# Kernel optimization log

Hardware: AMD Instinct MI355X
Metric: run time of the kernel (lower is better)

## Reference

```python
import jax, jax.numpy as jnp
import numpy as np

B, NVIS, NHID, NCLASS = 2048, 2048, 1024, 64


def setup_inputs() -> dict:
    key = jax.random.key(0)
    k1, k2, k3, k4, k5 = jax.random.split(key, 5)
    return {
        "v": jax.random.normal(k1, (B, NVIS), dtype=jnp.float32),
        "W": jax.random.normal(k2, (NVIS, NHID), dtype=jnp.float32),
        "c": jax.random.normal(k3, (1, NHID), dtype=jnp.float32),
        "d": jax.random.normal(k4, (1, NCLASS), dtype=jnp.float32),
        "U": jax.random.normal(k5, (NCLASS, NHID), dtype=jnp.float32),
    }


def reference(v, W, c, d, U):
    # precomputed_factor: [B, nhid]
    pre = jnp.matmul(v, W) + c
    # class free energies F[b, y] = d[0, y] + sum_j softplus(pre[b, j] + U[y, j])
    # broadcast to [B, nclass, nhid], reduce over hidden units
    F = d[0] + jnp.sum(jax.nn.softplus(pre[:, None, :] + U[None, :, :]), axis=-1)  # [B, nclass]
    # pairwise normalization 1 / sum_d exp(F_d - F_c) == softmax(F) along classes
    class_probs = jax.nn.softmax(F, axis=1)
    max_idx = jnp.argmax(class_probs, axis=1)
    one_hot = jax.nn.one_hot(max_idx, U.shape[0], dtype=jnp.int32)
    return class_probs, one_hot
```

## Files before the change

kernel.cpp:

```cpp
#include <hip/hip_runtime.h>

constexpr int kB    = 2048;
constexpr int kVIS  = 2048;
constexpr int kHID  = 1024;
constexpr int kCLS  = 64;
constexpr float kLog2e = 1.4426950408889634f;

typedef __attribute__((ext_vector_type(8))) short bf16x8;
typedef __attribute__((ext_vector_type(4))) float f32x4;

__device__ __forceinline__ unsigned short f2bf(float x) {
    unsigned u = __float_as_uint(x);
    u += 0x7fffu + ((u >> 16) & 1u);
    return (unsigned short)(u >> 16);
}
__device__ __forceinline__ float bf2f(unsigned short h) {
    return __uint_as_float(((unsigned)h) << 16);
}

__global__ __launch_bounds__(256) void prep_all(const float* __restrict__ v,
                                                const float* __restrict__ W,
                                                const float* __restrict__ U,
                                                unsigned short* __restrict__ vh,
                                                unsigned short* __restrict__ vl,
                                                unsigned short* __restrict__ wth,
                                                unsigned short* __restrict__ wtl,
                                                float* __restrict__ Ut) {
    __shared__ float T[32][33];
    const int bx = blockIdx.x;
    if (bx < 4096) {
        const int i = (bx * 256 + threadIdx.x) * 4;
        const float4 xv = *(const float4*)(v + i);
        ushort4 h, l;
        h.x = f2bf(xv.x); l.x = f2bf(xv.x - bf2f(h.x));
        h.y = f2bf(xv.y); l.y = f2bf(xv.y - bf2f(h.y));
        h.z = f2bf(xv.z); l.z = f2bf(xv.z - bf2f(h.z));
        h.w = f2bf(xv.w); l.w = f2bf(xv.w - bf2f(h.w));
        *(ushort4*)(vh + i) = h;
        *(ushort4*)(vl + i) = l;
    } else if (bx < 6144) {
        const int b = bx - 4096;
        const int n0 = (b & 31) * 32, k0 = (b >> 5) * 32;
        const int c = threadIdx.x & 31, r0 = threadIdx.x >> 5;
#pragma unroll
        for (int p = 0; p < 4; ++p) {
            const int r = r0 + p * 8;
            T[r][c] = W[(size_t)(k0 + r) * kHID + n0 + c];
        }
        __syncthreads();
#pragma unroll
        for (int p = 0; p < 4; ++p) {
            const int rr = r0 + p * 8;
            const float x = T[c][rr];
            const unsigned short h = f2bf(x);
            const unsigned short l = f2bf(x - bf2f(h));
            const size_t o = (size_t)(n0 + rr) * kVIS + k0 + c;
            wth[o] = h;
            wtl[o] = l;
        }
    } else {
        const int id = (bx - 6144) * 256 + threadIdx.x;
        const int j = id >> 6, y = id & 63;
        Ut[id] = U[(size_t)y * kHID + j] * kLog2e;
    }
}

constexpr int LDK = 72;

__global__ __launch_bounds__(256) void gemm_fused(const unsigned short* __restrict__ vh,
                                                  const unsigned short* __restrict__ vl,
                                                  const unsigned short* __restrict__ wth,
                                                  const unsigned short* __restrict__ wtl,
                                                  const float* __restrict__ cvec,
                                                  const float* __restrict__ Ut,
                                                  float* __restrict__ Fpart) {
    __shared__ __align__(16) union SMem {
        unsigned short stage[4][64 * LDK];
        struct { float ps[64][64]; float uts[64][64]; } epi;
    } smem;
    unsigned short* Ah = smem.stage[0];
    unsigned short* Al = smem.stage[1];
    unsigned short* Bh = smem.stage[2];
    unsigned short* Bl = smem.stage[3];

    const int tid = threadIdx.x;
    const int lane = tid & 63, wave = tid >> 6;
    const int m0 = blockIdx.y * 64, n0 = blockIdx.x * 64;
    const int wm = (wave >> 1) * 32, wn = (wave & 1) * 32;

    const int r0 = tid >> 3, r1 = r0 + 32;
    const int cg = (tid & 7) * 8;
    const size_t ga0 = (size_t)(m0 + r0) * kVIS + cg;
    const size_t ga1 = (size_t)(m0 + r1) * kVIS + cg;
    const size_t gb0 = (size_t)(n0 + r0) * kVIS + cg;
    const size_t gb1 = (size_t)(n0 + r1) * kVIS + cg;
    const int l0 = r0 * LDK + cg, l1 = r1 * LDK + cg;

    const int fm = lane & 15, fq = lane >> 4;
    const int fa0 = (wm + fm) * LDK + fq * 8;
    const int fa1 = (wm + 16 + fm) * LDK + fq * 8;
    const int fb0 = (wn + fm) * LDK + fq * 8;
    const int fb1 = (wn + 16 + fm) * LDK + fq * 8;

    f32x4 acc[2][2] = {};

    for (int k0 = 0; k0 < kVIS; k0 += 64) {
        const bf16x8 rah0 = *(const bf16x8*)(vh + ga0 + k0);
        const bf16x8 rah1 = *(const bf16x8*)(vh + ga1 + k0);
        const bf16x8 ral0 = *(const bf16x8*)(vl + ga0 + k0);
        const bf16x8 ral1 = *(const bf16x8*)(vl + ga1 + k0);
        const bf16x8 rbh0 = *(const bf16x8*)(wth + gb0 + k0);
        const bf16x8 rbh1 = *(const bf16x8*)(wth + gb1 + k0);
        const bf16x8 rbl0 = *(const bf16x8*)(wtl + gb0 + k0);
        const bf16x8 rbl1 = *(const bf16x8*)(wtl + gb1 + k0);
        __syncthreads();
        *(bf16x8*)(Ah + l0) = rah0; *(bf16x8*)(Ah + l1) = rah1;
        *(bf16x8*)(Al + l0) = ral0; *(bf16x8*)(Al + l1) = ral1;
        *(bf16x8*)(Bh + l0) = rbh0; *(bf16x8*)(Bh + l1) = rbh1;
        *(bf16x8*)(Bl + l0) = rbl0; *(bf16x8*)(Bl + l1) = rbl1;
        __syncthreads();
#pragma unroll
        for (int kk = 0; kk < 64; kk += 32) {
            const bf16x8 ah0 = *(const bf16x8*)(Ah + fa0 + kk);
            const bf16x8 ah1 = *(const bf16x8*)(Ah + fa1 + kk);
            const bf16x8 al0 = *(const bf16x8*)(Al + fa0 + kk);
            const bf16x8 al1 = *(const bf16x8*)(Al + fa1 + kk);
            const bf16x8 bh0 = *(const bf16x8*)(Bh + fb0 + kk);
            const bf16x8 bh1 = *(const bf16x8*)(Bh + fb1 + kk);
            const bf16x8 bl0 = *(const bf16x8*)(Bl + fb0 + kk);
            const bf16x8 bl1 = *(const bf16x8*)(Bl + fb1 + kk);
            acc[0][0] = __builtin_amdgcn_mfma_f32_16x16x32_bf16(ah0, bh0, acc[0][0], 0, 0, 0);
            acc[0][0] = __builtin_amdgcn_mfma_f32_16x16x32_bf16(ah0, bl0, acc[0][0], 0, 0, 0);
            acc[0][0] = __builtin_amdgcn_mfma_f32_16x16x32_bf16(al0, bh0, acc[0][0], 0, 0, 0);
            acc[0][1] = __builtin_amdgcn_mfma_f32_16x16x32_bf16(ah0, bh1, acc[0][1], 0, 0, 0);
            acc[0][1] = __builtin_amdgcn_mfma_f32_16x16x32_bf16(ah0, bl1, acc[0][1], 0, 0, 0);
            acc[0][1] = __builtin_amdgcn_mfma_f32_16x16x32_bf16(al0, bh1, acc[0][1], 0, 0, 0);
            acc[1][0] = __builtin_amdgcn_mfma_f32_16x16x32_bf16(ah1, bh0, acc[1][0], 0, 0, 0);
            acc[1][0] = __builtin_amdgcn_mfma_f32_16x16x32_bf16(ah1, bl0, acc[1][0], 0, 0, 0);
            acc[1][0] = __builtin_amdgcn_mfma_f32_16x16x32_bf16(al1, bh0, acc[1][0], 0, 0, 0);
            acc[1][1] = __builtin_amdgcn_mfma_f32_16x16x32_bf16(ah1, bh1, acc[1][1], 0, 0, 0);
            acc[1][1] = __builtin_amdgcn_mfma_f32_16x16x32_bf16(ah1, bl1, acc[1][1], 0, 0, 0);
            acc[1][1] = __builtin_amdgcn_mfma_f32_16x16x32_bf16(al1, bh1, acc[1][1], 0, 0, 0);
        }
    }

    __syncthreads();
#pragma unroll
    for (int j = 0; j < 2; ++j) {
        const int col = wn + j * 16 + fm;
        const float cv = cvec[n0 + col];
#pragma unroll
        for (int i = 0; i < 2; ++i) {
            const int rbase = wm + i * 16 + fq * 4;
#pragma unroll
            for (int r = 0; r < 4; ++r)
                smem.epi.ps[rbase + r][col] = (acc[i][j][r] + cv) * kLog2e;
        }
    }
    {
        const float4* src = (const float4*)(Ut + (size_t)n0 * kCLS);
        float4* dst = (float4*)smem.epi.uts;
        for (int i = tid; i < 64 * 64 / 4; i += 256) dst[i] = src[i];
    }
    __syncthreads();

    for (int rr = 0; rr < 16; ++rr) {
        const int row = wave * 16 + rr;
        float relu = 0.f;
        float prod = 1.f;
#pragma unroll 16
        for (int jj = 0; jj < 64; ++jj) {
            const float t = smem.epi.ps[row][jj] + smem.epi.uts[jj][lane];
            const float e = __builtin_amdgcn_exp2f(-fabsf(t));
            prod = __builtin_fmaf(prod, e, prod);
            relu += fmaxf(t, 0.f);
        }
        const float contrib = relu + __builtin_amdgcn_logf(prod);
        Fpart[((size_t)blockIdx.x * kB + m0 + row) * kCLS + lane] = contrib;
    }
}

__global__ __launch_bounds__(256) void softmax_final(const float* __restrict__ Fpart,
                                                     const float* __restrict__ dvec,
                                                     float* __restrict__ out) {
    const int tid = threadIdx.x;
    const int lane = tid & 63, wave = tid >> 6;
    const int row = blockIdx.x * 4 + wave;
    double s = 0.0;
#pragma unroll
    for (int k = 0; k < kHID / 64; ++k)
        s += (double)Fpart[((size_t)k * kB + row) * kCLS + lane];
    const float G = (float)s + dvec[lane] * kLog2e;

    float m = G;
    int mi = lane;
#pragma unroll
    for (int off = 32; off; off >>= 1) {
        const float om = __shfl_xor(m, off);
        const int   oi = __shfl_xor(mi, off);
        if (om > m || (om == m && oi < mi)) { m = om; mi = oi; }
    }
    const float e2 = __builtin_amdgcn_exp2f(G - m);
    float ssum = e2;
#pragma unroll
    for (int off = 32; off; off >>= 1) ssum += __shfl_xor(ssum, off);
    out[(size_t)row * kCLS + lane] = e2 / ssum;
    out[(size_t)kB * kCLS + (size_t)row * kCLS + lane] = (lane == mi) ? 1.0f : 0.0f;
}

constexpr int BM = 64, BN = 64, BK = 16;

__global__ __launch_bounds__(256) void gemm_vw(const float* __restrict__ V,
                                               const float* __restrict__ Wm,
                                               const float* __restrict__ cvec,
                                               float* __restrict__ pre) {
    __shared__ float As[BK][BM + 4];
    __shared__ float Bs[BK][BN + 4];
    const int tid = threadIdx.x;
    const int tx = tid & 15, ty = tid >> 4;
    const int m0 = blockIdx.y * BM, n0 = blockIdx.x * BN;
    const int arow = tid >> 2, acol = (tid & 3) << 2;
    const int brow = tid >> 4, bcol = (tid & 15) << 2;
    const float* vptr = V + (size_t)(m0 + arow) * kVIS + acol;
    const float* wptr = Wm + (size_t)brow * kHID + n0 + bcol;
    float acc[4][4] = {};
    for (int k0 = 0; k0 < kVIS; k0 += BK) {
        const float4 a4 = *(const float4*)(vptr + k0);
        const float4 b4 = *(const float4*)(wptr + (size_t)k0 * kHID);
        __syncthreads();
        As[acol + 0][arow] = a4.x; As[acol + 1][arow] = a4.y;
        As[acol + 2][arow] = a4.z; As[acol + 3][arow] = a4.w;
        *(float4*)&Bs[brow][bcol] = b4;
        __syncthreads();
#pragma unroll
        for (int k = 0; k < BK; ++k) {
            const float4 av = *(const float4*)&As[k][ty << 2];
            const float4 bv = *(const float4*)&Bs[k][tx << 2];
            const float a[4] = {av.x, av.y, av.z, av.w};
            const float b[4] = {bv.x, bv.y, bv.z, bv.w};
#pragma unroll
            for (int i = 0; i < 4; ++i)
#pragma unroll
                for (int j = 0; j < 4; ++j) acc[i][j] += a[i] * b[j];
        }
    }
#pragma unroll
    for (int i = 0; i < 4; ++i) {
        const int row = m0 + (ty << 2) + i;
        const int col = n0 + (tx << 2);
        const float4 cv = *(const float4*)(cvec + col);
        float4 o;
        o.x = acc[i][0] + cv.x; o.y = acc[i][1] + cv.y;
        o.z = acc[i][2] + cv.z; o.w = acc[i][3] + cv.w;
        *(float4*)(pre + (size_t)row * kHID + col) = o;
    }
}

__device__ __forceinline__ float softplus_f(float x) {
    return fmaxf(x, 0.f) + __logf(1.f + __expf(-fabsf(x)));
}

__global__ __launch_bounds__(256) void classify(const float* __restrict__ pre,
                                                const float* __restrict__ U,
                                                const float* __restrict__ dvec,
                                                float* __restrict__ out) {
    __shared__ float preS[4][kHID];
    __shared__ float Fs[4][kCLS];
    const int tid = threadIdx.x;
    const int lane = tid & 63, wave = tid >> 6;
    const int b0 = blockIdx.x * 4;
    const float4* src = (const float4*)(pre + (size_t)b0 * kHID);
    float4* dst = (float4*)preS;
    for (int i = tid; i < kHID; i += 256) dst[i] = src[i];
    __syncthreads();
    for (int yi = 0; yi < 16; ++yi) {
        const int y = (wave << 4) + yi;
        const float* Uy = U + (size_t)y * kHID;
        float a0 = 0.f, a1 = 0.f, a2 = 0.f, a3 = 0.f;
#pragma unroll
        for (int it = 0; it < kHID / 64; ++it) {
            const int j = lane + (it << 6);
            const float u = Uy[j];
            a0 += softplus_f(preS[0][j] + u);
            a1 += softplus_f(preS[1][j] + u);
            a2 += softplus_f(preS[2][j] + u);
            a3 += softplus_f(preS[3][j] + u);
        }
        double d0 = a0, d1 = a1, d2 = a2, d3 = a3;
#pragma unroll
        for (int off = 32; off; off >>= 1) {
            d0 += __shfl_xor(d0, off); d1 += __shfl_xor(d1, off);
            d2 += __shfl_xor(d2, off); d3 += __shfl_xor(d3, off);
        }
        if (lane == 0) {
            const float dy = dvec[y];
            Fs[0][y] = (float)d0 + dy; Fs[1][y] = (float)d1 + dy;
            Fs[2][y] = (float)d2 + dy; Fs[3][y] = (float)d3 + dy;
        }
    }
    __syncthreads();
    const float F = Fs[wave][lane];
    float m = F; int mi = lane;
#pragma unroll
    for (int off = 32; off; off >>= 1) {
        const float om = __shfl_xor(m, off);
        const int oi = __shfl_xor(mi, off);
        if (om > m || (om == m && oi < mi)) { m = om; mi = oi; }
    }
    const float e = __expf(F - m);
    float s = e;
#pragma unroll
    for (int off = 32; off; off >>= 1) s += __shfl_xor(s, off);
    const int row = b0 + wave;
    out[(size_t)row * kCLS + lane] = e / s;
    out[(size_t)kB * kCLS + (size_t)row * kCLS + lane] = (lane == mi) ? 1.0f : 0.0f;
}

extern "C" void kernel_launch(void* const* d_in, const int* in_sizes, int n_in,
                              void* d_out, int out_size, void* d_ws, size_t ws_size,
                              hipStream_t stream) {
    const float* v = (const float*)d_in[0];
    const float* W = (const float*)d_in[1];
    const float* c = (const float*)d_in[2];
    const float* d = (const float*)d_in[3];
    const float* U = (const float*)d_in[4];
    float* out = (float*)d_out;
    char* ws = (char*)d_ws;

    const size_t need = 33816576;
    if (ws_size >= need) {
        unsigned short* vh  = (unsigned short*)(ws);
        unsigned short* vl  = (unsigned short*)(ws + 8388608);
        unsigned short* wth = (unsigned short*)(ws + 16777216);
        unsigned short* wtl = (unsigned short*)(ws + 20971520);
        float* Ut    = (float*)(ws + 25165824);
        float* Fpart = (float*)(ws + 25427968);
        prep_all<<<6400, 256, 0, stream>>>(v, W, U, vh, vl, wth, wtl, Ut);
        gemm_fused<<<dim3(kHID / 64, kB / 64), 256, 0, stream>>>(vh, vl, wth, wtl, c, Ut, Fpart);
        softmax_final<<<kB / 4, 256, 0, stream>>>(Fpart, d, out);
    } else {
        float* pre = (float*)ws;
        gemm_vw<<<dim3(kHID / BN, kB / BM), 256, 0, stream>>>(v, W, c, pre);
        classify<<<kB / 4, 256, 0, stream>>>(pre, U, d, out);
    }
}
```

Baseline: 144.1 us.

## Load GEMM tiles via direct global-to-LDS with XOR swizzle; register-tile epilogue

Replaces the register-staged global loads plus LDS stores with global_load_lds direct transfers into an unpadded, XOR-swizzled LDS layout, and adjusts the MFMA fragment reads to match the swizzle. The epilogue now keeps U values in registers across 16 rows and reads the pre-activation tile as float4 from a padded LDS array, dropping the separate U staging into shared memory. This is meant to cut VGPR pressure, LDS instruction count and bank conflicts. In exchange it risks correctness if the global_load_lds per-lane addressing does not match the swizzled layout, and it raises register use in the epilogue.

```diff
diff --git a/kernel.cpp b/kernel.cpp
--- a/kernel.cpp
+++ b/kernel.cpp
@@ -8,6 +8,13 @@
 
 typedef __attribute__((ext_vector_type(8))) short bf16x8;
 typedef __attribute__((ext_vector_type(4))) float f32x4;
+
+typedef __attribute__((address_space(3))) unsigned       as3_u32;
+typedef __attribute__((address_space(1))) const unsigned as1_u32;
+
+__device__ __forceinline__ void g2lds16(const void* g, void* l) {
+    __builtin_amdgcn_global_load_lds((as1_u32*)g, (as3_u32*)l, 16, 0, 0);
+}
 
 __device__ __forceinline__ unsigned short f2bf(float x) {
     unsigned u = __float_as_uint(x);
@@ -65,8 +72,6 @@
     }
 }
 
-constexpr int LDK = 72;
-
 __global__ __launch_bounds__(256) void gemm_fused(const unsigned short* __restrict__ vh,
                                                   const unsigned short* __restrict__ vl,
                                                   const unsigned short* __restrict__ wth,
@@ -75,8 +80,8 @@
                                                   const float* __restrict__ Ut,
                                                   float* __restrict__ Fpart) {
     __shared__ __align__(16) union SMem {
-        unsigned short stage[4][64 * LDK];
-        struct { float ps[64][64]; float uts[64][64]; } epi;
+        unsigned short stage[4][64 * 64];
+        float ps[64][68];
     } smem;
     unsigned short* Ah = smem.stage[0];
     unsigned short* Al = smem.stage[1];
@@ -89,46 +94,43 @@
     const int wm = (wave >> 1) * 32, wn = (wave & 1) * 32;
 
     const int r0 = tid >> 3, r1 = r0 + 32;
-    const int cg = (tid & 7) * 8;
-    const size_t ga0 = (size_t)(m0 + r0) * kVIS + cg;
-    const size_t ga1 = (size_t)(m0 + r1) * kVIS + cg;
-    const size_t gb0 = (size_t)(n0 + r0) * kVIS + cg;
-    const size_t gb1 = (size_t)(n0 + r1) * kVIS + cg;
-    const int l0 = r0 * LDK + cg, l1 = r1 * LDK + cg;
+    const int oc = (((tid & 7) ^ ((tid >> 3) & 7)) << 3);
+    const size_t ga0 = (size_t)(m0 + r0) * kVIS + oc;
+    const size_t ga1 = (size_t)(m0 + r1) * kVIS + oc;
+    const size_t gb0 = (size_t)(n0 + r0) * kVIS + oc;
+    const size_t gb1 = (size_t)(n0 + r1) * kVIS + oc;
+    const int l0 = (r0 << 6) + ((tid & 7) << 3);
+    const int l1 = (r1 << 6) + ((tid & 7) << 3);
 
     const int fm = lane & 15, fq = lane >> 4;
-    const int fa0 = (wm + fm) * LDK + fq * 8;
-    const int fa1 = (wm + 16 + fm) * LDK + fq * 8;
-    const int fb0 = (wn + fm) * LDK + fq * 8;
-    const int fb1 = (wn + 16 + fm) * LDK + fq * 8;
+    const int rx = fm & 7;
+    const int a0r = (wm + fm) << 6,  a1r = (wm + 16 + fm) << 6;
+    const int b0r = (wn + fm) << 6,  b1r = (wn + 16 + fm) << 6;
 
     f32x4 acc[2][2] = {};
 
     for (int k0 = 0; k0 < kVIS; k0 += 64) {
-        const bf16x8 rah0 = *(const bf16x8*)(vh + ga0 + k0);
-        const bf16x8 rah1 = *(const bf16x8*)(vh + ga1 + k0);
-        const bf16x8 ral0 = *(const bf16x8*)(vl + ga0 + k0);
-        const bf16x8 ral1 = *(const bf16x8*)(vl + ga1 + k0);
-        const bf16x8 rbh0 = *(const bf16x8*)(wth + gb0 + k0);
-        const bf16x8 rbh1 = *(const bf16x8*)(wth + gb1 + k0);
-        const bf16x8 rbl0 = *(const bf16x8*)(wtl + gb0 + k0);
-        const bf16x8 rbl1 = *(const bf16x8*)(wtl + gb1 + k0);
-        __syncthreads();
-        *(bf16x8*)(Ah + l0) = rah0; *(bf16x8*)(Ah + l1) = rah1;
-        *(bf16x8*)(Al + l0) = ral0; *(bf16x8*)(Al + l1) = ral1;
-        *(bf16x8*)(Bh + l0) = rbh0; *(bf16x8*)(Bh + l1) = rbh1;
-        *(bf16x8*)(Bl + l0) = rbl0; *(bf16x8*)(Bl + l1) = rbl1;
+        __syncthreads();
+        g2lds16(vh + ga0 + k0, Ah + l0);
+        g2lds16(vh + ga1 + k0, Ah + l1);
+        g2lds16(vl + ga0 + k0, Al + l0);
+        g2lds16(vl + ga1 + k0, Al + l1);
+        g2lds16(wth + gb0 + k0, Bh + l0);
+        g2lds16(wth + gb1 + k0, Bh + l1);
+        g2lds16(wtl + gb0 + k0, Bl + l0);
+        g2lds16(wtl + gb1 + k0, Bl + l1);
         __syncthreads();
 #pragma unroll
         for (int kk = 0; kk < 64; kk += 32) {
-            const bf16x8 ah0 = *(const bf16x8*)(Ah + fa0 + kk);
-            const bf16x8 ah1 = *(const bf16x8*)(Ah + fa1 + kk);
-            const bf16x8 al0 = *(const bf16x8*)(Al + fa0 + kk);
-            const bf16x8 al1 = *(const bf16x8*)(Al + fa1 + kk);
-            const bf16x8 bh0 = *(const bf16x8*)(Bh + fb0 + kk);
-            const bf16x8 bh1 = *(const bf16x8*)(Bh + fb1 + kk);
-            const bf16x8 bl0 = *(const bf16x8*)(Bl + fb0 + kk);
-            const bf16x8 bl1 = *(const bf16x8*)(Bl + fb1 + kk);
+            const int p = (((kk >> 3) + fq) ^ rx) << 3;
+            const bf16x8 ah0 = *(const bf16x8*)(Ah + a0r + p);
+            const bf16x8 ah1 = *(const bf16x8*)(Ah + a1r + p);
+            const bf16x8 al0 = *(const bf16x8*)(Al + a0r + p);
+            const bf16x8 al1 = *(const bf16x8*)(Al + a1r + p);
+            const bf16x8 bh0 = *(const bf16x8*)(Bh + b0r + p);
+            const bf16x8 bh1 = *(const bf16x8*)(Bh + b1r + p);
+            const bf16x8 bl0 = *(const bf16x8*)(Bl + b0r + p);
+            const bf16x8 bl1 = *(const bf16x8*)(Bl + b1r + p);
             acc[0][0] = __builtin_amdgcn_mfma_f32_16x16x32_bf16(ah0, bh0, acc[0][0], 0, 0, 0);
             acc[0][0] = __builtin_amdgcn_mfma_f32_16x16x32_bf16(ah0, bl0, acc[0][0], 0, 0, 0);
             acc[0][0] = __builtin_amdgcn_mfma_f32_16x16x32_bf16(al0, bh0, acc[0][0], 0, 0, 0);
@@ -154,29 +156,38 @@
             const int rbase = wm + i * 16 + fq * 4;
 #pragma unroll
             for (int r = 0; r < 4; ++r)
-                smem.epi.ps[rbase + r][col] = (acc[i][j][r] + cv) * kLog2e;
-        }
-    }
-    {
-        const float4* src = (const float4*)(Ut + (size_t)n0 * kCLS);
-        float4* dst = (float4*)smem.epi.uts;
-        for (int i = tid; i < 64 * 64 / 4; i += 256) dst[i] = src[i];
+                smem.ps[rbase + r][col] = (acc[i][j][r] + cv) * kLog2e;
+        }
     }
     __syncthreads();
 
+    const float* UtN = Ut + (size_t)n0 * kCLS;
+    float relu[16], prod[16];
+#pragma unroll
+    for (int rr = 0; rr < 16; ++rr) { relu[rr] = 0.f; prod[rr] = 1.f; }
+
+    for (int jc = 0; jc < 64; jc += 8) {
+        float u[8];
+#pragma unroll
+        for (int q = 0; q < 8; ++q) u[q] = UtN[(jc + q) * kCLS + lane];
+#pragma unroll
+        for (int rr = 0; rr < 16; ++rr) {
+            const float4 p0 = *(const float4*)&smem.ps[wave * 16 + rr][jc];
+            const float4 p1 = *(const float4*)&smem.ps[wave * 16 + rr][jc + 4];
+            const float pv[8] = {p0.x, p0.y, p0.z, p0.w, p1.x, p1.y, p1.z, p1.w};
+#pragma unroll
+            for (int q = 0; q < 8; ++q) {
+                const float t = pv[q] + u[q];
+                const float e = __builtin_amdgcn_exp2f(-fabsf(t));
+                prod[rr] = __builtin_fmaf(prod[rr], e, prod[rr]);
+                relu[rr] += fmaxf(t, 0.f);
+            }
+        }
+    }
+#pragma unroll
     for (int rr = 0; rr < 16; ++rr) {
-        const int row = wave * 16 + rr;
-        float relu = 0.f;
-        float prod = 1.f;
-#pragma unroll 16
-        for (int jj = 0; jj < 64; ++jj) {
-            const float t = smem.epi.ps[row][jj] + smem.epi.uts[jj][lane];
-            const float e = __builtin_amdgcn_exp2f(-fabsf(t));
-            prod = __builtin_fmaf(prod, e, prod);
-            relu += fmaxf(t, 0.f);
-        }
-        const float contrib = relu + __builtin_amdgcn_logf(prod);
-        Fpart[((size_t)blockIdx.x * kB + m0 + row) * kCLS + lane] = contrib;
+        const float contrib = relu[rr] + __builtin_amdgcn_logf(prod[rr]);
+        Fpart[((size_t)blockIdx.x * kB + m0 + wave * 16 + rr) * kCLS + lane] = contrib;
     }
 }
 
```

Measured after the change: 136.0 us. 5.6% less time.
